# Performance work log

Measured on AMD Instinct MI355X. Metric: run time of the kernel, lower is better.

The kernel has to match this reference:

```python
import jax, jax.numpy as jnp
import numpy as np
from jax import lax

THRESHOLD = 0.8
EPS = 1e-3


def _conv2d_same(x, w, b):
    # x: [B,H,W,Cin], w: [3,3,Cin,Cout], b: [Cout]
    y = lax.conv_general_dilated(x, w, window_strides=(1, 1), padding='SAME',
                                 dimension_numbers=('NHWC', 'HWIO', 'NHWC'))
    return y + b


def _region_moments(x, flag):
    # x: [B,H,W,C], flag: [B,H,W,1] in {0,1}
    flag_sum = jnp.sum(jnp.sign(flag), axis=(1, 2), keepdims=True) + EPS
    mu = jnp.sum(x * flag, axis=(1, 2), keepdims=True) / flag_sum
    sigma = jnp.sum((x - mu) ** 2 * flag, axis=(1, 2), keepdims=True) / flag_sum
    return mu, sigma


def setup_inputs() -> dict:
    key = jax.random.key(0)
    k = jax.random.split(key, 4)
    B, H, W, C = 8, 256, 256, 128
    inputs = jax.random.normal(k[0], (B, H, W, C), dtype=jnp.float32)
    w_sr = jax.random.normal(k[1], (3, 3, 2, 1), dtype=jnp.float32) * 0.3
    w_gamma = jax.random.normal(k[2], (3, 3, 1, 1), dtype=jnp.float32) * 0.3
    w_beta = jax.random.normal(k[3], (3, 3, 1, 1), dtype=jnp.float32) * 0.3
    return {
        'inputs': inputs,
        'w_sr': w_sr, 'b_sr': jnp.zeros((1,), jnp.float32),
        'w_gamma': w_gamma, 'b_gamma': jnp.zeros((1,), jnp.float32),
        'w_beta': w_beta, 'b_beta': jnp.zeros((1,), jnp.float32),
    }


def reference(inputs, w_sr, b_sr, w_gamma, b_gamma, w_beta, b_beta):
    maxpool = jnp.max(inputs, axis=-1, keepdims=True)
    avgpool = jnp.mean(inputs, axis=-1, keepdims=True)
    x = jnp.concatenate([maxpool, avgpool], axis=-1)  # [B,H,W,2]
    x = jax.nn.sigmoid(_conv2d_same(x, w_sr, b_sr))   # [B,H,W,1]
    region_mask = jnp.sign(jax.nn.relu(x - THRESHOLD))  # {0,1}

    beta = _conv2d_same(x, w_beta, b_beta)
    gamma = _conv2d_same(x, w_gamma, b_gamma)

    mu_v, sig_v = _region_moments(inputs, region_mask)
    x_valid = (inputs - mu_v) / jnp.sqrt(sig_v + EPS) * region_mask

    inv_mask = 1.0 - region_mask
    mu_m, sig_m = _region_moments(inputs, inv_mask)
    x_mask = (inputs - mu_m) / jnp.sqrt(sig_m + EPS) * inv_mask

    out = x_valid + x_mask
    return out * beta + gamma
```

## Files before the change

kernel.cpp:

```cpp
#include <hip/hip_runtime.h>

#define BB 8
#define HH 256
#define WW 256
#define CC 128
#define HW (HH*WW)
#define NP (BB*HW)
#define THRESHOLD 0.8f
#define EPSV 1e-3f

__global__ __launch_bounds__(256) void k_pool(const float* __restrict__ in,
                                              float2* __restrict__ pooled) {
    int p    = blockIdx.x * 4 + (threadIdx.x >> 6);
    int lane = threadIdx.x & 63;
    const float2 v = *reinterpret_cast<const float2*>(in + (size_t)p * CC + lane * 2);
    float mx = fmaxf(v.x, v.y);
    float sm = v.x + v.y;
#pragma unroll
    for (int m = 32; m >= 1; m >>= 1) {
        mx = fmaxf(mx, __shfl_xor(mx, m));
        sm += __shfl_xor(sm, m);
    }
    if (lane == 0) pooled[p] = make_float2(mx, sm * (1.0f / 128.0f));
}

__global__ __launch_bounds__(256) void k_conv_sr(const float2* __restrict__ pooled,
                                                 const float* __restrict__ w_sr,
                                                 const float* __restrict__ b_sr,
                                                 float* __restrict__ x,
                                                 float* __restrict__ mask) {
    int p = blockIdx.x * 256 + threadIdx.x;
    int b = p >> 16;
    int hw = p & 65535;
    int h = hw >> 8, w = hw & 255;
    float acc = b_sr[0];
#pragma unroll
    for (int kh = 0; kh < 3; ++kh) {
        int hh = h + kh - 1;
        if ((unsigned)hh >= HH) continue;
#pragma unroll
        for (int kw = 0; kw < 3; ++kw) {
            int ww = w + kw - 1;
            if ((unsigned)ww >= WW) continue;
            float2 pv = pooled[(size_t)b * HW + hh * WW + ww];
            acc += pv.x * w_sr[(kh * 3 + kw) * 2 + 0] + pv.y * w_sr[(kh * 3 + kw) * 2 + 1];
        }
    }
    float s = 1.0f / (1.0f + expf(-acc));
    x[p] = s;
    mask[p] = (s > THRESHOLD) ? 1.0f : 0.0f;
}

__global__ __launch_bounds__(256) void k_conv_gb(const float* __restrict__ x,
                                                 const float* __restrict__ w_gamma,
                                                 const float* __restrict__ b_gamma,
                                                 const float* __restrict__ w_beta,
                                                 const float* __restrict__ b_beta,
                                                 float* __restrict__ gamma,
                                                 float* __restrict__ beta) {
    int p = blockIdx.x * 256 + threadIdx.x;
    int b = p >> 16;
    int hw = p & 65535;
    int h = hw >> 8, w = hw & 255;
    float ag = b_gamma[0], ab = b_beta[0];
#pragma unroll
    for (int kh = 0; kh < 3; ++kh) {
        int hh = h + kh - 1;
        if ((unsigned)hh >= HH) continue;
#pragma unroll
        for (int kw = 0; kw < 3; ++kw) {
            int ww = w + kw - 1;
            if ((unsigned)ww >= WW) continue;
            float xv = x[(size_t)b * HW + hh * WW + ww];
            ag += xv * w_gamma[kh * 3 + kw];
            ab += xv * w_beta[kh * 3 + kw];
        }
    }
    gamma[p] = ag;
    beta[p] = ab;
}

__global__ __launch_bounds__(256) void k_moments(const float* __restrict__ in,
                                                 const float* __restrict__ mask,
                                                 float* __restrict__ acc,
                                                 float* __restrict__ cnt) {
    int b     = blockIdx.x >> 8;
    int chunk = blockIdx.x & 255;
    int tid   = threadIdx.x;
    int c     = tid & 127;
    int half  = tid >> 7;
    float s_v = 0.f, ss_v = 0.f, s_m = 0.f, ss_m = 0.f, cv = 0.f;
    int base = chunk * 256;
    for (int i = 0; i < 128; ++i) {
        int pl = base + i * 2 + half;
        size_t p = (size_t)b * HW + pl;
        float m = mask[p];
        float v = in[p * CC + c];
        float v2 = v * v;
        if (m > 0.5f) { s_v += v; ss_v += v2; }
        else          { s_m += v; ss_m += v2; }
        cv += m;
    }
    __shared__ float sh[5][256];
    sh[0][tid] = s_v; sh[1][tid] = ss_v; sh[2][tid] = s_m; sh[3][tid] = ss_m; sh[4][tid] = cv;
    __syncthreads();
    if (tid < 128) {
        atomicAdd(&acc[0 * 1024 + b * 128 + tid], sh[0][tid] + sh[0][tid + 128]);
        atomicAdd(&acc[1 * 1024 + b * 128 + tid], sh[1][tid] + sh[1][tid + 128]);
        atomicAdd(&acc[2 * 1024 + b * 128 + tid], sh[2][tid] + sh[2][tid + 128]);
        atomicAdd(&acc[3 * 1024 + b * 128 + tid], sh[3][tid] + sh[3][tid + 128]);
    }
    if (tid == 0) atomicAdd(&cnt[b], sh[4][0] + sh[4][128]);
}

__global__ void k_stats(const float* __restrict__ acc, const float* __restrict__ cnt,
                        float* __restrict__ stats) {
    int i = blockIdx.x * 256 + threadIdx.x;
    if (i >= 1024) return;
    int b = i >> 7;
    float cv = cnt[b];
    float cm = (float)HW - cv;
    float s_v = acc[i], ss_v = acc[1024 + i], s_m = acc[2048 + i], ss_m = acc[3072 + i];
    float fs_v = cv + EPSV;
    float mu_v = s_v / fs_v;
    float sig_v = (ss_v - 2.f * mu_v * s_v + mu_v * mu_v * cv) / fs_v;
    float fs_m = cm + EPSV;
    float mu_m = s_m / fs_m;
    float sig_m = (ss_m - 2.f * mu_m * s_m + mu_m * mu_m * cm) / fs_m;
    stats[i]        = mu_v;
    stats[1024 + i] = 1.0f / sqrtf(sig_v + EPSV);
    stats[2048 + i] = mu_m;
    stats[3072 + i] = 1.0f / sqrtf(sig_m + EPSV);
}

__global__ __launch_bounds__(256) void k_apply(const float* __restrict__ in,
                                               const float* __restrict__ mask,
                                               const float* __restrict__ beta,
                                               const float* __restrict__ gamma,
                                               const float* __restrict__ stats,
                                               float* __restrict__ out) {
    size_t idx = (size_t)blockIdx.x * 256 + threadIdx.x;
    size_t p = idx >> 5;
    int c4 = (int)(idx & 31);
    int b = (int)(p >> 16);
    const float4 v = reinterpret_cast<const float4*>(in)[idx];
    float m  = mask[p];
    float be = beta[p];
    float ga = gamma[p];
    int si = b * 128 + c4 * 4;
    float4 mu, rs;
    if (m > 0.5f) {
        mu = *reinterpret_cast<const float4*>(stats + si);
        rs = *reinterpret_cast<const float4*>(stats + 1024 + si);
    } else {
        mu = *reinterpret_cast<const float4*>(stats + 2048 + si);
        rs = *reinterpret_cast<const float4*>(stats + 3072 + si);
    }
    float4 o;
    o.x = (v.x - mu.x) * rs.x * be + ga;
    o.y = (v.y - mu.y) * rs.y * be + ga;
    o.z = (v.z - mu.z) * rs.z * be + ga;
    o.w = (v.w - mu.w) * rs.w * be + ga;
    reinterpret_cast<float4*>(out)[idx] = o;
}

extern "C" void kernel_launch(void* const* d_in, const int* in_sizes, int n_in,
                              void* d_out, int out_size, void* d_ws, size_t ws_size,
                              hipStream_t stream) {
    const float* in      = (const float*)d_in[0];
    const float* w_sr    = (const float*)d_in[1];
    const float* b_sr    = (const float*)d_in[2];
    const float* w_gamma = (const float*)d_in[3];
    const float* b_gamma = (const float*)d_in[4];
    const float* w_beta  = (const float*)d_in[5];
    const float* b_beta  = (const float*)d_in[6];
    float* out = (float*)d_out;
    float* ws  = (float*)d_ws;

    float2* pooled = (float2*)ws;
    float* x     = ws + 2 * (size_t)NP;
    float* mask  = ws + 3 * (size_t)NP;
    float* beta  = ws + 4 * (size_t)NP;
    float* gamma = ws + 5 * (size_t)NP;
    float* acc   = ws + 6 * (size_t)NP;
    float* cnt   = acc + 4096;
    float* stats = cnt + 8;

    hipMemsetAsync(acc, 0, (4096 + 8) * sizeof(float), stream);

    k_pool   <<<NP / 4,  256, 0, stream>>>(in, pooled);
    k_conv_sr<<<NP / 256, 256, 0, stream>>>(pooled, w_sr, b_sr, x, mask);
    k_conv_gb<<<NP / 256, 256, 0, stream>>>(x, w_gamma, b_gamma, w_beta, b_beta, gamma, beta);
    k_moments<<<BB * 256, 256, 0, stream>>>(in, mask, acc, cnt);
    k_stats  <<<4, 256, 0, stream>>>(acc, cnt, stats);
    k_apply  <<<(NP * (size_t)CC / 4) / 256, 256, 0, stream>>>(in, mask, beta, gamma, stats, out);
}
```

Baseline: 577.7 us.

## Fuse sigmoid conv and gamma/beta convs into tiled shared-memory kernel, vectorize moments

```diff
diff --git a/kernel.cpp b/kernel.cpp
--- a/kernel.cpp
+++ b/kernel.cpp
@@ -10,7 +10,11 @@
 #define EPSV 1e-3f
 
 __global__ __launch_bounds__(256) void k_pool(const float* __restrict__ in,
-                                              float2* __restrict__ pooled) {
+                                              float2* __restrict__ pooled,
+                                              float* __restrict__ zbuf) {
+    if (blockIdx.x == 0) {
+        for (int i = threadIdx.x; i < 4104; i += 256) zbuf[i] = 0.0f;
+    }
     int p    = blockIdx.x * 4 + (threadIdx.x >> 6);
     int lane = threadIdx.x & 63;
     const float2 v = *reinterpret_cast<const float2*>(in + (size_t)p * CC + lane * 2);
@@ -24,93 +28,120 @@
     if (lane == 0) pooled[p] = make_float2(mx, sm * (1.0f / 128.0f));
 }
 
-__global__ __launch_bounds__(256) void k_conv_sr(const float2* __restrict__ pooled,
-                                                 const float* __restrict__ w_sr,
-                                                 const float* __restrict__ b_sr,
-                                                 float* __restrict__ x,
-                                                 float* __restrict__ mask) {
-    int p = blockIdx.x * 256 + threadIdx.x;
-    int b = p >> 16;
-    int hw = p & 65535;
-    int h = hw >> 8, w = hw & 255;
-    float acc = b_sr[0];
-#pragma unroll
-    for (int kh = 0; kh < 3; ++kh) {
-        int hh = h + kh - 1;
-        if ((unsigned)hh >= HH) continue;
-#pragma unroll
-        for (int kw = 0; kw < 3; ++kw) {
-            int ww = w + kw - 1;
-            if ((unsigned)ww >= WW) continue;
-            float2 pv = pooled[(size_t)b * HW + hh * WW + ww];
-            acc += pv.x * w_sr[(kh * 3 + kw) * 2 + 0] + pv.y * w_sr[(kh * 3 + kw) * 2 + 1];
+__global__ __launch_bounds__(256) void k_mask(const float2* __restrict__ pooled,
+                                              const float* __restrict__ w_sr,
+                                              const float* __restrict__ b_sr,
+                                              const float* __restrict__ w_gamma,
+                                              const float* __restrict__ b_gamma,
+                                              const float* __restrict__ w_beta,
+                                              const float* __restrict__ b_beta,
+                                              float* __restrict__ mask,
+                                              float2* __restrict__ bg,
+                                              float* __restrict__ cnt) {
+    int b    = blockIdx.x >> 6;
+    int tile = blockIdx.x & 63;
+    int th0  = (tile >> 3) * 32;
+    int tw0  = (tile & 7) * 32;
+    __shared__ float xs[34][35];
+    __shared__ float csh;
+    if (threadIdx.x == 0) csh = 0.0f;
+
+    float wsr[18], wg[9], wb[9];
+#pragma unroll
+    for (int i = 0; i < 18; ++i) wsr[i] = w_sr[i];
+#pragma unroll
+    for (int i = 0; i < 9; ++i) { wg[i] = w_gamma[i]; wb[i] = w_beta[i]; }
+    float bsr = b_sr[0], bg0 = b_gamma[0], bb0 = b_beta[0];
+
+    for (int i = threadIdx.x; i < 34 * 34; i += 256) {
+        int ly = i / 34, lx = i - ly * 34;
+        int h = th0 + ly - 1, w = tw0 + lx - 1;
+        float val = 0.0f;
+        if ((unsigned)h < HH && (unsigned)w < WW) {
+            float acc = bsr;
+#pragma unroll
+            for (int kh = 0; kh < 3; ++kh) {
+                int hh = h + kh - 1;
+                if ((unsigned)hh >= HH) continue;
+#pragma unroll
+                for (int kw = 0; kw < 3; ++kw) {
+                    int ww = w + kw - 1;
+                    if ((unsigned)ww >= WW) continue;
+                    float2 pv = pooled[(size_t)b * HW + hh * WW + ww];
+                    acc += pv.x * wsr[(kh * 3 + kw) * 2 + 0] + pv.y * wsr[(kh * 3 + kw) * 2 + 1];
+                }
+            }
+            val = 1.0f / (1.0f + expf(-acc));
         }
-    }
-    float s = 1.0f / (1.0f + expf(-acc));
-    x[p] = s;
-    mask[p] = (s > THRESHOLD) ? 1.0f : 0.0f;
-}
-
-__global__ __launch_bounds__(256) void k_conv_gb(const float* __restrict__ x,
-                                                 const float* __restrict__ w_gamma,
-                                                 const float* __restrict__ b_gamma,
-                                                 const float* __restrict__ w_beta,
-                                                 const float* __restrict__ b_beta,
-                                                 float* __restrict__ gamma,
-                                                 float* __restrict__ beta) {
-    int p = blockIdx.x * 256 + threadIdx.x;
-    int b = p >> 16;
-    int hw = p & 65535;
-    int h = hw >> 8, w = hw & 255;
-    float ag = b_gamma[0], ab = b_beta[0];
-#pragma unroll
-    for (int kh = 0; kh < 3; ++kh) {
-        int hh = h + kh - 1;
-        if ((unsigned)hh >= HH) continue;
-#pragma unroll
-        for (int kw = 0; kw < 3; ++kw) {
-            int ww = w + kw - 1;
-            if ((unsigned)ww >= WW) continue;
-            float xv = x[(size_t)b * HW + hh * WW + ww];
-            ag += xv * w_gamma[kh * 3 + kw];
-            ab += xv * w_beta[kh * 3 + kw];
-        }
-    }
-    gamma[p] = ag;
-    beta[p] = ab;
+        xs[ly][lx] = val;
+    }
+    __syncthreads();
+
+    float csum = 0.0f;
+    for (int i = threadIdx.x; i < 1024; i += 256) {
+        int ty = i >> 5, tx = i & 31;
+        float xc = xs[ty + 1][tx + 1];
+        float m = (xc > THRESHOLD) ? 1.0f : 0.0f;
+        csum += m;
+        float ag = bg0, ab = bb0;
+#pragma unroll
+        for (int kh = 0; kh < 3; ++kh)
+#pragma unroll
+            for (int kw = 0; kw < 3; ++kw) {
+                float xv = xs[ty + kh][tx + kw];
+                ag += xv * wg[kh * 3 + kw];
+                ab += xv * wb[kh * 3 + kw];
+            }
+        size_t p = (size_t)b * HW + (size_t)(th0 + ty) * WW + (tw0 + tx);
+        mask[p] = m;
+        bg[p] = make_float2(ab, ag);
+    }
+    atomicAdd(&csh, csum);
+    __syncthreads();
+    if (threadIdx.x == 0) atomicAdd(&cnt[b], csh);
 }
 
 __global__ __launch_bounds__(256) void k_moments(const float* __restrict__ in,
                                                  const float* __restrict__ mask,
-                                                 float* __restrict__ acc,
-                                                 float* __restrict__ cnt) {
-    int b     = blockIdx.x >> 8;
-    int chunk = blockIdx.x & 255;
-    int tid   = threadIdx.x;
-    int c     = tid & 127;
-    int half  = tid >> 7;
-    float s_v = 0.f, ss_v = 0.f, s_m = 0.f, ss_m = 0.f, cv = 0.f;
-    int base = chunk * 256;
-    for (int i = 0; i < 128; ++i) {
-        int pl = base + i * 2 + half;
+                                                 float* __restrict__ acc) {
+    int b     = blockIdx.x >> 7;
+    int chunk = blockIdx.x & 127;
+    int c4    = threadIdx.x & 31;
+    int pg    = threadIdx.x >> 5;
+    float4 sv = make_float4(0, 0, 0, 0), ssv = sv, sm = sv, ssm = sv;
+    int pbase = chunk * 512;
+    for (int i = 0; i < 64; ++i) {
+        int pl = pbase + i * 8 + pg;
         size_t p = (size_t)b * HW + pl;
         float m = mask[p];
-        float v = in[p * CC + c];
-        float v2 = v * v;
-        if (m > 0.5f) { s_v += v; ss_v += v2; }
-        else          { s_m += v; ss_m += v2; }
-        cv += m;
-    }
-    __shared__ float sh[5][256];
-    sh[0][tid] = s_v; sh[1][tid] = ss_v; sh[2][tid] = s_m; sh[3][tid] = ss_m; sh[4][tid] = cv;
+        const float4 v = *reinterpret_cast<const float4*>(in + p * CC + c4 * 4);
+        float4 v2 = make_float4(v.x * v.x, v.y * v.y, v.z * v.z, v.w * v.w);
+        if (m > 0.5f) {
+            sv.x += v.x; sv.y += v.y; sv.z += v.z; sv.w += v.w;
+            ssv.x += v2.x; ssv.y += v2.y; ssv.z += v2.z; ssv.w += v2.w;
+        } else {
+            sm.x += v.x; sm.y += v.y; sm.z += v.z; sm.w += v.w;
+            ssm.x += v2.x; ssm.y += v2.y; ssm.z += v2.z; ssm.w += v2.w;
+        }
+    }
+    __shared__ float4 sh[4][8][32];
+    sh[0][pg][c4] = sv; sh[1][pg][c4] = ssv; sh[2][pg][c4] = sm; sh[3][pg][c4] = ssm;
     __syncthreads();
-    if (tid < 128) {
-        atomicAdd(&acc[0 * 1024 + b * 128 + tid], sh[0][tid] + sh[0][tid + 128]);
-        atomicAdd(&acc[1 * 1024 + b * 128 + tid], sh[1][tid] + sh[1][tid + 128]);
-        atomicAdd(&acc[2 * 1024 + b * 128 + tid], sh[2][tid] + sh[2][tid + 128]);
-        atomicAdd(&acc[3 * 1024 + b * 128 + tid], sh[3][tid] + sh[3][tid + 128]);
-    }
-    if (tid == 0) atomicAdd(&cnt[b], sh[4][0] + sh[4][128]);
+    int t = threadIdx.x;
+    if (t < 128) {
+        int arr = t >> 5, c = t & 31;
+        float4 s = sh[arr][0][c];
+#pragma unroll
+        for (int j = 1; j < 8; ++j) {
+            float4 u = sh[arr][j][c];
+            s.x += u.x; s.y += u.y; s.z += u.z; s.w += u.w;
+        }
+        float* dst = acc + arr * 1024 + b * 128 + c * 4;
+        atomicAdd(dst + 0, s.x);
+        atomicAdd(dst + 1, s.y);
+        atomicAdd(dst + 2, s.z);
+        atomicAdd(dst + 3, s.w);
+    }
 }
 
 __global__ void k_stats(const float* __restrict__ acc, const float* __restrict__ cnt,
@@ -135,8 +166,7 @@
 
 __global__ __launch_bounds__(256) void k_apply(const float* __restrict__ in,
                                                const float* __restrict__ mask,
-                                               const float* __restrict__ beta,
-                                               const float* __restrict__ gamma,
+                                               const float2* __restrict__ bg,
                                                const float* __restrict__ stats,
                                                float* __restrict__ out) {
     size_t idx = (size_t)blockIdx.x * 256 + threadIdx.x;
@@ -144,18 +174,13 @@
     int c4 = (int)(idx & 31);
     int b = (int)(p >> 16);
     const float4 v = reinterpret_cast<const float4*>(in)[idx];
-    float m  = mask[p];
-    float be = beta[p];
-    float ga = gamma[p];
-    int si = b * 128 + c4 * 4;
-    float4 mu, rs;
-    if (m > 0.5f) {
-        mu = *reinterpret_cast<const float4*>(stats + si);
-        rs = *reinterpret_cast<const float4*>(stats + 1024 + si);
-    } else {
-        mu = *reinterpret_cast<const float4*>(stats + 2048 + si);
-        rs = *reinterpret_cast<const float4*>(stats + 3072 + si);
-    }
+    float m   = mask[p];
+    float2 bgv = bg[p];
+    float be = bgv.x, ga = bgv.y;
+    int off = (m > 0.5f) ? 0 : 2048;
+    int si = off + b * 128 + c4 * 4;
+    const float4 mu = *reinterpret_cast<const float4*>(stats + si);
+    const float4 rs = *reinterpret_cast<const float4*>(stats + si + 1024);
     float4 o;
     o.x = (v.x - mu.x) * rs.x * be + ga;
     o.y = (v.y - mu.y) * rs.y * be + ga;
@@ -178,20 +203,16 @@
     float* ws  = (float*)d_ws;
 
     float2* pooled = (float2*)ws;
-    float* x     = ws + 2 * (size_t)NP;
-    float* mask  = ws + 3 * (size_t)NP;
-    float* beta  = ws + 4 * (size_t)NP;
-    float* gamma = ws + 5 * (size_t)NP;
-    float* acc   = ws + 6 * (size_t)NP;
-    float* cnt   = acc + 4096;
-    float* stats = cnt + 8;
-
-    hipMemsetAsync(acc, 0, (4096 + 8) * sizeof(float), stream);
-
-    k_pool   <<<NP / 4,  256, 0, stream>>>(in, pooled);
-    k_conv_sr<<<NP / 256, 256, 0, stream>>>(pooled, w_sr, b_sr, x, mask);
-    k_conv_gb<<<NP / 256, 256, 0, stream>>>(x, w_gamma, b_gamma, w_beta, b_beta, gamma, beta);
-    k_moments<<<BB * 256, 256, 0, stream>>>(in, mask, acc, cnt);
+    float*  mask   = ws + 2 * (size_t)NP;
+    float2* bg     = (float2*)(ws + 3 * (size_t)NP);
+    float*  acc    = ws + 5 * (size_t)NP;
+    float*  cnt    = acc + 4096;
+    float*  stats  = cnt + 8;
+
+    k_pool   <<<NP / 4,  256, 0, stream>>>(in, pooled, acc);
+    k_mask   <<<BB * 64, 256, 0, stream>>>(pooled, w_sr, b_sr, w_gamma, b_gamma,
+                                           w_beta, b_beta, mask, bg, cnt);
+    k_moments<<<BB * 128, 256, 0, stream>>>(in, mask, acc);
     k_stats  <<<4, 256, 0, stream>>>(acc, cnt, stats);
-    k_apply  <<<(NP * (size_t)CC / 4) / 256, 256, 0, stream>>>(in, mask, beta, gamma, stats, out);
-}
+    k_apply  <<<(int)((size_t)NP * CC / 4 / 256), 256, 0, stream>>>(in, mask, bg, stats, out);
+}
```

Result: no change. 580.8 us (+0.5%).
